# Kernel optimization log

Measured on AMD Instinct MI355X. Metric: run time of the kernel, lower is better.

The kernel has to match this reference:

```python
import jax, jax.numpy as jnp
import numpy as np

ALPHA = 0.2            # LeakyReLU negative slope
NEG_BIG = -9e15        # mask fill value from the original code


def setup_inputs() -> dict:
    key = jax.random.key(0)
    k1, k2, k3, k4 = jax.random.split(key, 4)
    N, F_in, F_out = 8192, 512, 256
    x = jax.random.normal(k1, (N, F_in), dtype=jnp.float32)
    support = jax.random.randint(k2, (N, N), 0, 2, dtype=jnp.int32)  # dense 0/1 adjacency
    W = jax.random.normal(k3, (F_in, F_out), dtype=jnp.float32) * (1.0 / np.sqrt(F_in))
    a = jax.random.normal(k4, (2 * F_out, 1), dtype=jnp.float32) * 0.05
    return {"x": x, "support": support, "W": W, "a": a}


def _attention_logits(h, a):
    # Faithful reproduction of the ORIGINAL (buggy) torch layout:
    #   a_input = cat([h.repeat(1,N).view(N*N,-1), h.repeat(N,1)], dim=0).view(N, N, 2F)
    # Working out the flat-index arithmetic (N even):
    #   for i <  N/2: a_input[i,j] = concat(h[q], h[q]),  q = 2*i + (j >= N/2)
    #   for i >= N/2: a_input[i,j] = concat(h[(2j) % N], h[(2j+1) % N])   (independent of i)
    # so e_raw[i,j] = a_input[i,j] @ a decomposes via s = h@a1, t = h@a2.
    N, F = h.shape
    a1 = a[:F, 0]
    a2 = a[F:, 0]
    s = h @ a1                     # (N,)
    t = h @ a2                     # (N,)
    u = s + t
    half = N // 2
    j = jnp.arange(N)
    i_top = jnp.arange(half)
    q = 2 * i_top[:, None] + (j[None, :] >= half).astype(jnp.int32)  # (half, N)
    top = u[q]                                                       # rows i < N/2
    bot = s[(2 * j) % N] + t[(2 * j + 1) % N]                        # (N,) same for all i >= N/2
    e_raw = jnp.concatenate([top, jnp.broadcast_to(bot, (N - half, N))], axis=0)
    return jnp.where(e_raw > 0, e_raw, ALPHA * e_raw)  # LeakyReLU


def reference(x, support, W, a):
    h = x @ W                                  # (N, F_out)
    e = _attention_logits(h, a)                # (N, N)
    scores = jnp.where(support > 0, e, jnp.float32(NEG_BIG))
    attn = jax.nn.softmax(scores, axis=1)      # dropout p=0.0 -> identity
    h_out = attn @ h                           # (N, F_out)
    return jax.nn.elu(h_out)                   # concat=True
```

## Files before the change

### kernel.cpp

```cpp
#include <hip/hip_runtime.h>


typedef short bf16x8 __attribute__((ext_vector_type(8)));
typedef float f32x4 __attribute__((ext_vector_type(4)));

static __device__ __forceinline__ unsigned short f2bf(float f) {
    unsigned int u = __builtin_bit_cast(unsigned int, f);
    unsigned int r = (u + 0x7FFFu + ((u >> 16) & 1u)) >> 16;
    return (unsigned short)r;
}
static __device__ __forceinline__ float bf2f(unsigned short s) {
    unsigned int u = ((unsigned int)s) << 16;
    return __builtin_bit_cast(float, u);
}
static __device__ __forceinline__ void glds16(const unsigned short* g, unsigned short* l) {
    __builtin_amdgcn_global_load_lds(
        (const __attribute__((address_space(1))) unsigned int*)(g),
        (__attribute__((address_space(3))) unsigned int*)(l), 16, 0, 0);
}

__global__ __launch_bounds__(256) void k_cvt_x(const float* __restrict__ x,
                                               unsigned short* __restrict__ xb) {
    int i = (blockIdx.x * 256 + threadIdx.x) * 4;
    float4 v = *(const float4*)(x + i);
    ushort4 o = make_ushort4(f2bf(v.x), f2bf(v.y), f2bf(v.z), f2bf(v.w));
    *(ushort4*)(xb + i) = o;
}

__global__ __launch_bounds__(256) void k_cvt_w(const float* __restrict__ W,
                                               unsigned short* __restrict__ Wbt) {
    int idx = blockIdx.x * 256 + threadIdx.x;
    int n = idx >> 9, k = idx & 511;
    Wbt[idx] = f2bf(W[k * 256 + n]);
}

__global__ __launch_bounds__(256) void k_gemm_h(const unsigned short* __restrict__ xb,
                                                const unsigned short* __restrict__ Wbt,
                                                unsigned short* __restrict__ h,
                                                unsigned short* __restrict__ B1t) {
    __shared__ unsigned short Asm[128][72];
    __shared__ unsigned short Bsm[64][72];
    int tid = threadIdx.x;
    int wv = tid >> 6, ln = tid & 63;
    int m0 = blockIdx.x * 128, n0 = blockIdx.y * 64;

    f32x4 acc[2][4];
#pragma unroll
    for (int i = 0; i < 2; i++)
#pragma unroll
        for (int j = 0; j < 4; j++) acc[i][j] = (f32x4)0.0f;

    for (int k0 = 0; k0 < 512; k0 += 64) {
        {
            int r = tid >> 1, c = (tid & 1) * 32;
            const unsigned short* src = xb + (m0 + r) * 512 + k0 + c;
            *(bf16x8*)&Asm[r][c]      = *(const bf16x8*)(src);
            *(bf16x8*)&Asm[r][c + 8]  = *(const bf16x8*)(src + 8);
            *(bf16x8*)&Asm[r][c + 16] = *(const bf16x8*)(src + 16);
            *(bf16x8*)&Asm[r][c + 24] = *(const bf16x8*)(src + 24);
        }
        {
            int r = tid >> 2, c = (tid & 3) * 16;
            const unsigned short* src = Wbt + (n0 + r) * 512 + k0 + c;
            *(bf16x8*)&Bsm[r][c]     = *(const bf16x8*)(src);
            *(bf16x8*)&Bsm[r][c + 8] = *(const bf16x8*)(src + 8);
        }
        __syncthreads();
        int lr = ln & 15, lk = (ln >> 4) * 8;
#pragma unroll
        for (int ks = 0; ks < 2; ks++) {
            int kk = ks * 32 + lk;
            bf16x8 a0 = *(const bf16x8*)&Asm[wv * 32 + lr][kk];
            bf16x8 a1 = *(const bf16x8*)&Asm[wv * 32 + 16 + lr][kk];
#pragma unroll
            for (int nt = 0; nt < 4; nt++) {
                bf16x8 b = *(const bf16x8*)&Bsm[nt * 16 + lr][kk];
                acc[0][nt] = __builtin_amdgcn_mfma_f32_16x16x32_bf16(a0, b, acc[0][nt], 0, 0, 0);
                acc[1][nt] = __builtin_amdgcn_mfma_f32_16x16x32_bf16(a1, b, acc[1][nt], 0, 0, 0);
            }
        }
        __syncthreads();
    }
    int lr = ln & 15, lrow = (ln >> 4) * 4;
#pragma unroll
    for (int mt = 0; mt < 2; mt++) {
#pragma unroll
        for (int nt = 0; nt < 4; nt++) {
            int mg = m0 + wv * 32 + mt * 16 + lrow;
            int ng = n0 + nt * 16 + lr;
            ushort4 tb = make_ushort4(f2bf(acc[mt][nt][0]), f2bf(acc[mt][nt][1]),
                                      f2bf(acc[mt][nt][2]), f2bf(acc[mt][nt][3]));
            h[(mg + 0) * 256 + ng] = tb.x;
            h[(mg + 1) * 256 + ng] = tb.y;
            h[(mg + 2) * 256 + ng] = tb.z;
            h[(mg + 3) * 256 + ng] = tb.w;
            *(ushort4*)&B1t[ng * 8192 + mg] = tb;
        }
    }
}

__global__ __launch_bounds__(256) void k_st(const unsigned short* __restrict__ h,
                                            const float* __restrict__ a,
                                            float* __restrict__ s, float* __restrict__ t) {
    int wv = threadIdx.x >> 6, ln = threadIdx.x & 63;
    int j = blockIdx.x * 4 + wv;
    ushort4 hv = *(const ushort4*)(h + j * 256 + ln * 4);
    float4 a1 = *(const float4*)(a + ln * 4);
    float4 a2 = *(const float4*)(a + 256 + ln * 4);
    float s_ = bf2f(hv.x) * a1.x + bf2f(hv.y) * a1.y + bf2f(hv.z) * a1.z + bf2f(hv.w) * a1.w;
    float t_ = bf2f(hv.x) * a2.x + bf2f(hv.y) * a2.y + bf2f(hv.z) * a2.z + bf2f(hv.w) * a2.w;
#pragma unroll
    for (int off = 32; off; off >>= 1) {
        s_ += __shfl_down(s_, off);
        t_ += __shfl_down(t_, off);
    }
    if (ln == 0) { s[j] = s_; t[j] = t_; }
}

__global__ __launch_bounds__(256) void k_weights(const float* __restrict__ s,
                                                 const float* __restrict__ t,
                                                 float* __restrict__ wb,
                                                 float* __restrict__ eL,
                                                 float* __restrict__ eR,
                                                 unsigned short* __restrict__ B1t) {
    int j = blockIdx.x * 256 + threadIdx.x;
    float eb = s[(2 * j) & 8191] + t[(2 * j + 1) & 8191];
    eb = eb > 0.0f ? eb : 0.2f * eb;
    wb[j] = expf(eb);
    if (j < 4096) {
        float cL = s[2 * j] + t[2 * j];
        cL = cL > 0.0f ? cL : 0.2f * cL;
        float cR = s[2 * j + 1] + t[2 * j + 1];
        cR = cR > 0.0f ? cR : 0.2f * cR;
        eL[j] = expf(cL);
        eR[j] = expf(cR);
    }
    B1t[256 * 8192 + j] = 0x3F80;
#pragma unroll
    for (int f = 257; f < 272; f++) B1t[f * 8192 + j] = 0;
}

__global__ __launch_bounds__(256) void k_b2(const unsigned short* __restrict__ B1t,
                                            const float* __restrict__ wb,
                                            unsigned short* __restrict__ B2t) {
    int j = blockIdx.x * 256 + threadIdx.x;
    int f = blockIdx.y;
    B2t[f * 8192 + j] = f2bf(wb[j] * bf2f(B1t[f * 8192 + j]));
}

static __device__ __forceinline__ bf16x8 cvt01(int4 a, int4 b) {
    bf16x8 r;
    r[0] = a.x ? (short)0x3F80 : (short)0; r[1] = a.y ? (short)0x3F80 : (short)0;
    r[2] = a.z ? (short)0x3F80 : (short)0; r[3] = a.w ? (short)0x3F80 : (short)0;
    r[4] = b.x ? (short)0x3F80 : (short)0; r[5] = b.y ? (short)0x3F80 : (short)0;
    r[6] = b.z ? (short)0x3F80 : (short)0; r[7] = b.w ? (short)0x3F80 : (short)0;
    return r;
}

__global__ __launch_bounds__(256, 2) void k_mgemm(const int* __restrict__ sup,
                                                  const unsigned short* __restrict__ B1t,
                                                  const unsigned short* __restrict__ B2t,
                                                  float* __restrict__ P) {
    __shared__ unsigned short Bsm[4 * 8704];
    int tid = threadIdx.x, wv = tid >> 6, ln = tid & 63;
    int bid = blockIdx.x;
    int q = bid & 7;
    int strip = bid >> 3;
    long K0 = (long)q * 1024;
    long m0 = (long)strip * 128;
    const unsigned short* Bt = (strip < 32) ? B1t : B2t;

    const unsigned short* sp[5];
    int cb[5];
#pragma unroll
    for (int i = 0; i < 4; i++) {
        int ch = i * 256 + wv * 64 + ln;
        int row = ch >> 2, c = ch & 3;
        cb[i] = (i * 256 + wv * 64) * 8;
        sp[i] = Bt + (long)row * 8192 + K0 + ((c ^ (row & 3)) << 3);
    }
    {
        int ch = 1024 + wv * 16 + (ln & 15);
        int row = ch >> 2, c = ch & 3;
        cb[4] = (1024 + wv * 16) * 8;
        sp[4] = Bt + (long)row * 8192 + K0 + ((c ^ (row & 3)) << 3);
    }

    const int* ap0 = sup + (m0 + wv * 32 + (ln & 15)) * 8192 + K0 + (ln >> 4) * 8;
    const int* ap1 = ap0 + 16 * 8192;

    f32x4 acc[2][17];
#pragma unroll
    for (int i = 0; i < 2; i++)
#pragma unroll
        for (int j = 0; j < 17; j++) acc[i][j] = (f32x4)0.0f;

    int4 A[4][4];

#define STAGE_B(T, BUF) do {                                         \
        unsigned short* dst_ = Bsm + (BUF) * 8704;                   \
        long ko_ = (long)(T) * 32;                                   \
        glds16(sp[0] + ko_, dst_ + cb[0]);                           \
        glds16(sp[1] + ko_, dst_ + cb[1]);                           \
        glds16(sp[2] + ko_, dst_ + cb[2]);                           \
        glds16(sp[3] + ko_, dst_ + cb[3]);                           \
        if (ln < 16) glds16(sp[4] + ko_, dst_ + cb[4]);              \
    } while (0)

#define LOAD_A(T, S) do {                                            \
        const int* a0_ = ap0 + (long)(T) * 32;                       \
        const int* a1_ = ap1 + (long)(T) * 32;                       \
        A[S][0] = *(const int4*)(a0_); A[S][1] = *(const int4*)(a0_ + 4); \
        A[S][2] = *(const int4*)(a1_); A[S][3] = *(const int4*)(a1_ + 4); \
    } while (0)

#define MFMA_STEP(BUF, S) do {                                       \
        bf16x8 av0 = cvt01(A[S][0], A[S][1]);                        \
        bf16x8 av1 = cvt01(A[S][2], A[S][3]);                        \
        const char* base_ = (const char*)Bsm + (BUF) * 17408 + 64 * lr + swz16; \
        __builtin_amdgcn_s_setprio(1);                               \
        _Pragma("unroll")                                            \
        for (int f = 0; f < 17; f++) {                               \
            bf16x8 bv = *(const bf16x8*)(base_ + f * 1024);          \
            acc[0][f] = __builtin_amdgcn_mfma_f32_16x16x32_bf16(av0, bv, acc[0][f], 0, 0, 0); \
            acc[1][f] = __builtin_amdgcn_mfma_f32_16x16x32_bf16(av1, bv, acc[1][f], 0, 0, 0); \
        }                                                            \
        __builtin_amdgcn_s_setprio(0);                               \
    } while (0)

#define WB14() do { asm volatile("s_waitcnt vmcnt(14)" ::: "memory"); \
                    __builtin_amdgcn_s_barrier(); } while (0)

    int lr = ln & 15;
    int swz16 = 16 * ((ln >> 4) ^ (ln & 3));

    STAGE_B(0, 0);
    LOAD_A(0, 0);
    STAGE_B(1, 1);
    LOAD_A(1, 1);
    STAGE_B(2, 2);
    WB14();

#pragma unroll 1
    for (int t = 0; t < 28; t += 4) {
        LOAD_A(t + 2, 2); STAGE_B(t + 3, 3); MFMA_STEP(0, 0); WB14();
        LOAD_A(t + 3, 3); STAGE_B(t + 4, 0); MFMA_STEP(1, 1); WB14();
        LOAD_A(t + 4, 0); STAGE_B(t + 5, 1); MFMA_STEP(2, 2); WB14();
        LOAD_A(t + 5, 1); STAGE_B(t + 6, 2); MFMA_STEP(3, 3); WB14();
    }
    LOAD_A(30, 2); STAGE_B(31, 3); MFMA_STEP(0, 0); WB14();
    LOAD_A(31, 3);                 MFMA_STEP(1, 1);
    asm volatile("s_waitcnt vmcnt(9)" ::: "memory");
    __builtin_amdgcn_s_barrier();
    MFMA_STEP(2, 2);
    asm volatile("s_waitcnt vmcnt(0)" ::: "memory");
    __builtin_amdgcn_s_barrier();
    MFMA_STEP(3, 3);

#undef STAGE_B
#undef LOAD_A
#undef MFMA_STEP
#undef WB14

    long grow = m0 + wv * 32 + (ln >> 4) * 4;
    float* op = P + ((long)q * 8192 + grow) * 272 + lr;
#pragma unroll
    for (int mf = 0; mf < 2; mf++)
#pragma unroll
        for (int f = 0; f < 17; f++)
#pragma unroll
            for (int r = 0; r < 4; r++)
                op[(long)(mf * 16 + r) * 272 + f * 16] = acc[mf][f][r];
}

__global__ __launch_bounds__(256) void k_out(const float* __restrict__ P,
                                             const float* __restrict__ eL,
                                             const float* __restrict__ eR,
                                             float* __restrict__ outp) {
    int i = blockIdx.x, f = threadIdx.x;
    const float* p = P + (long)i * 272;
    const long QS = 8192l * 272;
    float num, den;
    if (i < 4096) {
        float tln = 0, trn = 0, tld = 0, trd = 0;
#pragma unroll
        for (int q = 0; q < 4; q++) { tln += p[q * QS + f]; tld += p[q * QS + 256]; }
#pragma unroll
        for (int q = 4; q < 8; q++) { trn += p[q * QS + f]; trd += p[q * QS + 256]; }
        float el = eL[i], er = eR[i];
        num = el * tln + er * trn;
        den = el * tld + er * trd;
    } else {
        num = 0; den = 0;
#pragma unroll
        for (int q = 0; q < 8; q++) { num += p[q * QS + f]; den += p[q * QS + 256]; }
    }
    float r = num / den;
    outp[(long)i * 256 + f] = r > 0.0f ? r : expm1f(r);
}

extern "C" void kernel_launch(void* const* d_in, const int* in_sizes, int n_in,
                              void* d_out, int out_size, void* d_ws, size_t ws_size,
                              hipStream_t stream) {
    (void)in_sizes; (void)n_in; (void)out_size; (void)ws_size;
    const float* x = (const float*)d_in[0];
    const int* sup = (const int*)d_in[1];
    const float* W = (const float*)d_in[2];
    const float* a = (const float*)d_in[3];
    float* outp = (float*)d_out;

    char* ws = (char*)d_ws;
    size_t off = 0;
    auto alloc = [&](size_t bytes) -> void* {
        void* p = ws + off;
        off += (bytes + 255) & ~(size_t)255;
        return p;
    };
    unsigned short* xb  = (unsigned short*)alloc(8192 * 512 * 2);
    unsigned short* Wbt = (unsigned short*)alloc(256 * 512 * 2);
    unsigned short* h   = (unsigned short*)alloc(8192 * 256 * 2);
    unsigned short* B1t = (unsigned short*)alloc(272 * 8192 * 2);
    unsigned short* B2t = (unsigned short*)alloc(272 * 8192 * 2);
    float* s   = (float*)alloc(8192 * 4);
    float* t   = (float*)alloc(8192 * 4);
    float* wb  = (float*)alloc(8192 * 4);
    float* eL  = (float*)alloc(4096 * 4);
    float* eR  = (float*)alloc(4096 * 4);
    float* P   = (float*)alloc((size_t)8 * 8192 * 272 * 4);

    k_cvt_x<<<4096, 256, 0, stream>>>(x, xb);
    k_cvt_w<<<512, 256, 0, stream>>>(W, Wbt);
    k_gemm_h<<<dim3(64, 4), 256, 0, stream>>>(xb, Wbt, h, B1t);
    k_st<<<2048, 256, 0, stream>>>(h, a, s, t);
    k_weights<<<32, 256, 0, stream>>>(s, t, wb, eL, eR, B1t);
    k_b2<<<dim3(32, 272), 256, 0, stream>>>(B1t, wb, B2t);
    k_mgemm<<<512, 256, 0, stream>>>(sup, B1t, B2t, P);
    k_out<<<8192, 256, 0, stream>>>(P, eL, eR, outp);
}
```

Before: 213.7 us.

## Pack int32 adjacency into bitmask before masked GEMM

```diff
diff --git a/kernel.cpp b/kernel.cpp
--- a/kernel.cpp
+++ b/kernel.cpp
@@ -17,6 +17,30 @@
     __builtin_amdgcn_global_load_lds(
         (const __attribute__((address_space(1))) unsigned int*)(g),
         (__attribute__((address_space(3))) unsigned int*)(l), 16, 0, 0);
+}
+static __device__ __forceinline__ bf16x8 expand_byte(unsigned int b) {
+    union { bf16x8 v; unsigned int u[4]; } r;
+#pragma unroll
+    for (int w = 0; w < 4; w++) {
+        unsigned int lo = (b >> (2 * w)) & 1u;
+        unsigned int hi = (b >> (2 * w + 1)) & 1u;
+        r.u[w] = (lo ? 0x3F80u : 0u) | (hi ? 0x3F800000u : 0u);
+    }
+    return r.v;
+}
+
+__global__ __launch_bounds__(256) void k_pack(const int* __restrict__ sup,
+                                              unsigned long long* __restrict__ bits) {
+    int wid = (blockIdx.x << 2) | (threadIdx.x >> 6);
+    int ln = threadIdx.x & 63;
+    const int* rp = sup + (long)wid * 8192 + ln;
+    unsigned long long* bp = bits + (long)wid * 128;
+#pragma unroll 4
+    for (int w = 0; w < 128; w++) {
+        int v = rp[(long)w * 64];
+        unsigned long long m = __ballot(v != 0);
+        if (ln == 0) bp[w] = m;
+    }
 }
 
 __global__ __launch_bounds__(256) void k_cvt_x(const float* __restrict__ x,
@@ -148,16 +172,7 @@
     B2t[f * 8192 + j] = f2bf(wb[j] * bf2f(B1t[f * 8192 + j]));
 }
 
-static __device__ __forceinline__ bf16x8 cvt01(int4 a, int4 b) {
-    bf16x8 r;
-    r[0] = a.x ? (short)0x3F80 : (short)0; r[1] = a.y ? (short)0x3F80 : (short)0;
-    r[2] = a.z ? (short)0x3F80 : (short)0; r[3] = a.w ? (short)0x3F80 : (short)0;
-    r[4] = b.x ? (short)0x3F80 : (short)0; r[5] = b.y ? (short)0x3F80 : (short)0;
-    r[6] = b.z ? (short)0x3F80 : (short)0; r[7] = b.w ? (short)0x3F80 : (short)0;
-    return r;
-}
-
-__global__ __launch_bounds__(256, 2) void k_mgemm(const int* __restrict__ sup,
+__global__ __launch_bounds__(256, 2) void k_mgemm(const unsigned char* __restrict__ bits,
                                                   const unsigned short* __restrict__ B1t,
                                                   const unsigned short* __restrict__ B2t,
                                                   float* __restrict__ P) {
@@ -186,8 +201,8 @@
         sp[4] = Bt + (long)row * 8192 + K0 + ((c ^ (row & 3)) << 3);
     }
 
-    const int* ap0 = sup + (m0 + wv * 32 + (ln & 15)) * 8192 + K0 + (ln >> 4) * 8;
-    const int* ap1 = ap0 + 16 * 8192;
+    const unsigned char* ap0 = bits + (m0 + wv * 32 + (ln & 15)) * 1024 + q * 128 + (ln >> 4);
+    const unsigned char* ap1 = ap0 + 16 * 1024;
 
     f32x4 acc[2][17];
 #pragma unroll
@@ -195,7 +210,7 @@
 #pragma unroll
         for (int j = 0; j < 17; j++) acc[i][j] = (f32x4)0.0f;
 
-    int4 A[4][4];
+    unsigned int ax0, ay0, ax1, ay1, ax2, ay2, ax3, ay3;
 
 #define STAGE_B(T, BUF) do {                                         \
         unsigned short* dst_ = Bsm + (BUF) * 8704;                   \
@@ -207,16 +222,14 @@
         if (ln < 16) glds16(sp[4] + ko_, dst_ + cb[4]);              \
     } while (0)
 
-#define LOAD_A(T, S) do {                                            \
-        const int* a0_ = ap0 + (long)(T) * 32;                       \
-        const int* a1_ = ap1 + (long)(T) * 32;                       \
-        A[S][0] = *(const int4*)(a0_); A[S][1] = *(const int4*)(a0_ + 4); \
-        A[S][2] = *(const int4*)(a1_); A[S][3] = *(const int4*)(a1_ + 4); \
+#define LOAD_AB(T, AX, AY) do {                                      \
+        AX = ap0[(T) * 4];                                           \
+        AY = ap1[(T) * 4];                                           \
     } while (0)
 
-#define MFMA_STEP(BUF, S) do {                                       \
-        bf16x8 av0 = cvt01(A[S][0], A[S][1]);                        \
-        bf16x8 av1 = cvt01(A[S][2], A[S][3]);                        \
+#define MSTEP(BUF, AX, AY) do {                                      \
+        bf16x8 av0 = expand_byte(AX);                                \
+        bf16x8 av1 = expand_byte(AY);                                \
         const char* base_ = (const char*)Bsm + (BUF) * 17408 + 64 * lr + swz16; \
         __builtin_amdgcn_s_setprio(1);                               \
         _Pragma("unroll")                                            \
@@ -228,39 +241,40 @@
         __builtin_amdgcn_s_setprio(0);                               \
     } while (0)
 
-#define WB14() do { asm volatile("s_waitcnt vmcnt(14)" ::: "memory"); \
-                    __builtin_amdgcn_s_barrier(); } while (0)
+#define WB(N) do { asm volatile("s_waitcnt vmcnt(" #N ")" ::: "memory"); \
+                   __builtin_amdgcn_s_barrier(); } while (0)
 
     int lr = ln & 15;
     int swz16 = 16 * ((ln >> 4) ^ (ln & 3));
 
+    LOAD_AB(0, ax0, ay0);
+    LOAD_AB(1, ax1, ay1);
     STAGE_B(0, 0);
-    LOAD_A(0, 0);
     STAGE_B(1, 1);
-    LOAD_A(1, 1);
     STAGE_B(2, 2);
-    WB14();
+    WB(10);
+
+    LOAD_AB(2, ax2, ay2); STAGE_B(3, 3); MSTEP(0, ax0, ay0); WB(12);
+    LOAD_AB(3, ax3, ay3); STAGE_B(4, 0); MSTEP(1, ax1, ay1); WB(14);
+    LOAD_AB(4, ax0, ay0); STAGE_B(5, 1); MSTEP(2, ax2, ay2); WB(14);
+    LOAD_AB(5, ax1, ay1); STAGE_B(6, 2); MSTEP(3, ax3, ay3); WB(14);
 
 #pragma unroll 1
-    for (int t = 0; t < 28; t += 4) {
-        LOAD_A(t + 2, 2); STAGE_B(t + 3, 3); MFMA_STEP(0, 0); WB14();
-        LOAD_A(t + 3, 3); STAGE_B(t + 4, 0); MFMA_STEP(1, 1); WB14();
-        LOAD_A(t + 4, 0); STAGE_B(t + 5, 1); MFMA_STEP(2, 2); WB14();
-        LOAD_A(t + 5, 1); STAGE_B(t + 6, 2); MFMA_STEP(3, 3); WB14();
-    }
-    LOAD_A(30, 2); STAGE_B(31, 3); MFMA_STEP(0, 0); WB14();
-    LOAD_A(31, 3);                 MFMA_STEP(1, 1);
-    asm volatile("s_waitcnt vmcnt(9)" ::: "memory");
-    __builtin_amdgcn_s_barrier();
-    MFMA_STEP(2, 2);
-    asm volatile("s_waitcnt vmcnt(0)" ::: "memory");
-    __builtin_amdgcn_s_barrier();
-    MFMA_STEP(3, 3);
+    for (int t = 4; t < 28; t += 4) {
+        LOAD_AB(t + 2, ax2, ay2); STAGE_B(t + 3, 3); MSTEP(0, ax0, ay0); WB(14);
+        LOAD_AB(t + 3, ax3, ay3); STAGE_B(t + 4, 0); MSTEP(1, ax1, ay1); WB(14);
+        LOAD_AB(t + 4, ax0, ay0); STAGE_B(t + 5, 1); MSTEP(2, ax2, ay2); WB(14);
+        LOAD_AB(t + 5, ax1, ay1); STAGE_B(t + 6, 2); MSTEP(3, ax3, ay3); WB(14);
+    }
+    LOAD_AB(30, ax2, ay2); STAGE_B(31, 3); MSTEP(0, ax0, ay0); WB(14);
+    LOAD_AB(31, ax3, ay3);                 MSTEP(1, ax1, ay1); WB(9);
+    MSTEP(2, ax2, ay2);                                        WB(0);
+    MSTEP(3, ax3, ay3);
 
 #undef STAGE_B
-#undef LOAD_A
-#undef MFMA_STEP
-#undef WB14
+#undef LOAD_AB
+#undef MSTEP
+#undef WB
 
     long grow = m0 + wv * 32 + (ln >> 4) * 4;
     float* op = P + ((long)q * 8192 + grow) * 272 + lr;
@@ -321,6 +335,7 @@
     unsigned short* h   = (unsigned short*)alloc(8192 * 256 * 2);
     unsigned short* B1t = (unsigned short*)alloc(272 * 8192 * 2);
     unsigned short* B2t = (unsigned short*)alloc(272 * 8192 * 2);
+    unsigned long long* bits = (unsigned long long*)alloc((size_t)8192 * 1024);
     float* s   = (float*)alloc(8192 * 4);
     float* t   = (float*)alloc(8192 * 4);
     float* wb  = (float*)alloc(8192 * 4);
@@ -328,12 +343,13 @@
     float* eR  = (float*)alloc(4096 * 4);
     float* P   = (float*)alloc((size_t)8 * 8192 * 272 * 4);
 
+    k_pack<<<2048, 256, 0, stream>>>(sup, bits);
     k_cvt_x<<<4096, 256, 0, stream>>>(x, xb);
     k_cvt_w<<<512, 256, 0, stream>>>(W, Wbt);
     k_gemm_h<<<dim3(64, 4), 256, 0, stream>>>(xb, Wbt, h, B1t);
     k_st<<<2048, 256, 0, stream>>>(h, a, s, t);
     k_weights<<<32, 256, 0, stream>>>(s, t, wb, eL, eR, B1t);
     k_b2<<<dim3(32, 272), 256, 0, stream>>>(B1t, wb, B2t);
-    k_mgemm<<<512, 256, 0, stream>>>(sup, B1t, B2t, P);
+    k_mgemm<<<512, 256, 0, stream>>>((const unsigned char*)bits, B1t, B2t, P);
     k_out<<<8192, 256, 0, stream>>>(P, eL, eR, outp);
 }
```

New measurement: 223.8 us. +4.7%, slower.
